# Performance work log

Hardware: AMD Instinct MI355X
Metric: run time of the kernel (lower is better)

## Reference

```python
import jax, jax.numpy as jnp
import numpy as np

N_NODES = 150000
N_ETYPES = 1000
B = 16384
D_CONT = 2
N_NCAT = 3
NCAT_CARD = 64
NCAT_DIM = 16
ETYPE_DIM = 32
N_ECAT = 2
ECAT_CARD = 32
ECAT_DIM = 16
T_DIM = 16
D_IN = D_CONT + N_NCAT * NCAT_DIM      # 50
H = 128                                 # gnn_hidden_dim
P_IN = 2 * H + ETYPE_DIM + N_ECAT * ECAT_DIM + T_DIM  # 336
P_HID = 64


def setup_inputs() -> dict:
    key = jax.random.key(0)
    ks = jax.random.split(key, 24)
    s = 0.05
    inp = {
        "src_node_ids": jax.random.randint(ks[0], (B,), 0, N_NODES),
        "dst_node_ids": jax.random.randint(ks[1], (B,), 0, N_NODES),
        "edge_type_ids": jax.random.randint(ks[2], (B,), 0, N_ETYPES),
        "t_rel": jax.random.uniform(ks[3], (B, 1), dtype=jnp.float32),
        "node_cont": jax.random.normal(ks[4], (N_NODES, D_CONT), dtype=jnp.float32),
        "node_cat_codes": jax.random.randint(ks[5], (N_NCAT, N_NODES), 0, NCAT_CARD),
        "edge_cat_codes": jax.random.randint(ks[6], (N_ECAT, N_ETYPES), 0, ECAT_CARD),
        "edge_index": jax.random.randint(ks[7], (2, 1500000), 0, N_NODES),
        "h_prev": jax.random.normal(ks[8], (N_NODES, H), dtype=jnp.float32),
        "c_prev": jax.random.normal(ks[9], (N_NODES, H), dtype=jnp.float32),
        # learned parameters
        "node_cat_emb": jax.random.normal(ks[10], (N_NCAT, NCAT_CARD, NCAT_DIM), dtype=jnp.float32) * s,
        "edge_id_emb": jax.random.normal(ks[11], (N_ETYPES, ETYPE_DIM), dtype=jnp.float32) * s,
        "edge_cat_emb": jax.random.normal(ks[12], (N_ECAT, ECAT_CARD, ECAT_DIM), dtype=jnp.float32) * s,
        "time_W": jax.random.normal(ks[13], (1, T_DIM), dtype=jnp.float32) * s,
        "time_b": jnp.zeros((T_DIM,), dtype=jnp.float32),
        # GConvLSTM (ChebConv K=1 per gate): gates ordered [i, f, c, o]
        "Wx": jax.random.normal(ks[14], (4, D_IN, H), dtype=jnp.float32) * s,
        "Wh": jax.random.normal(ks[15], (4, H, H), dtype=jnp.float32) * s,
        "b_gate": jnp.zeros((4, H), dtype=jnp.float32),
        "w_c": jax.random.normal(ks[16], (3, H), dtype=jnp.float32) * s,  # peephole for i, f, o
        "W1": jax.random.normal(ks[17], (P_IN, P_HID), dtype=jnp.float32) * s,
        "b1": jnp.zeros((P_HID,), dtype=jnp.float32),
        "W2": jax.random.normal(ks[18], (P_HID, 1), dtype=jnp.float32) * s,
        "b2": jnp.zeros((1,), dtype=jnp.float32),
    }
    return inp


def reference(src_node_ids, dst_node_ids, edge_type_ids, t_rel, node_cont,
              node_cat_codes, edge_cat_codes, edge_index, h_prev, c_prev,
              node_cat_emb, edge_id_emb, edge_cat_emb, time_W, time_b,
              Wx, Wh, b_gate, w_c, W1, b1, W2, b2):
    # --- process node features: cont + 3 categorical embedding gathers ---
    # node_cat_emb[f, node_cat_codes[f, n]] -> [N_NCAT, N, NCAT_DIM]
    cat_e = node_cat_emb[jnp.arange(N_NCAT)[:, None], node_cat_codes]
    cat_e = jnp.transpose(cat_e, (1, 0, 2)).reshape(N_NODES, N_NCAT * NCAT_DIM)
    x = jnp.concatenate([node_cont, cat_e], axis=-1)  # [N, D_IN]

    # --- process batch edge-type features ---
    eid_e = edge_id_emb[edge_type_ids]                               # [B, 32]
    codes_b = edge_cat_codes[:, edge_type_ids]                       # [N_ECAT, B]
    ecat_e = edge_cat_emb[jnp.arange(N_ECAT)[:, None], codes_b]      # [N_ECAT, B, 16]
    ecat_e = jnp.transpose(ecat_e, (1, 0, 2)).reshape(-1, N_ECAT * ECAT_DIM)
    edge_feat = jnp.concatenate([eid_e, ecat_e], axis=-1)            # [B, 64]

    # --- time encoding ---
    t = t_rel if t_rel.ndim == 2 else t_rel[:, None]
    time_e = t @ time_W + time_b                                     # [B, 16]

    # --- GConvLSTM step. ChebConv with K=1: out = x @ W0 + b (T_0(L)x = x),
    # so edge_index is mathematically unused. Gates: [i, f, c_tilde, o]. ---
    z = (jnp.einsum('nd,gdh->gnh', x, Wx)
         + jnp.einsum('nh,ghk->gnk', h_prev, Wh)
         + b_gate[:, None, :])                                       # [4, N, H]
    i_g = jax.nn.sigmoid(z[0] + w_c[0] * c_prev)
    f_g = jax.nn.sigmoid(z[1] + w_c[1] * c_prev)
    t_g = jnp.tanh(z[2])
    c_new = f_g * c_prev + i_g * t_g
    o_g = jax.nn.sigmoid(z[3] + w_c[2] * c_new)
    h_new = o_g * jnp.tanh(c_new)

    # --- link predictor ---
    src_e = h_new[src_node_ids]                                      # [B, H]
    dst_e = h_new[dst_node_ids]                                      # [B, H]
    comb = jnp.concatenate([src_e, dst_e, edge_feat, time_e], axis=-1)  # [B, 336]
    hid = jax.nn.relu(comb @ W1 + b1)
    prob = jax.nn.sigmoid(hid @ W2 + b2)[:, 0]                       # [B]
    return prob, h_new, c_new
```

## Files before the change

### kernel.cpp

```cpp
#include <hip/hip_runtime.h>

#define N_NODES   150000
#define N_PAD     150016
#define B_EDGES   16384
#define H         128
#define KP        192
#define N_NCAT    3
#define NCAT_CARD 64
#define NCAT_DIM  16
#define N_ETYPES  1000
#define ETYPE_DIM 32
#define N_ECAT    2
#define ECAT_CARD 32
#define ECAT_DIM  16
#define T_DIM     16
#define P_IN      336
#define P_HID     64

typedef __bf16 bf16x8 __attribute__((ext_vector_type(8)));
typedef float  f32x4  __attribute__((ext_vector_type(4)));

__device__ __forceinline__ float rcp_(float x)      { return __builtin_amdgcn_rcpf(x); }
__device__ __forceinline__ float sigmoidf_(float x) { return rcp_(1.0f + __expf(-x)); }
__device__ __forceinline__ float tanhf_(float x)    { return 1.0f - 2.0f * rcp_(__expf(2.0f * x) + 1.0f); }
__device__ __forceinline__ unsigned short f2bf(float f) {
    unsigned u = __float_as_uint(f);
    u += 0x7fffu + ((u >> 16) & 1u);
    return (unsigned short)(u >> 16);
}

__global__ __launch_bounds__(256) void build_a_kernel(
    const float* __restrict__ node_cont,
    const int*   __restrict__ node_cat_codes,
    const float* __restrict__ node_cat_emb,
    const float* __restrict__ h_prev,
    unsigned short* __restrict__ A)
{
    const int t = threadIdx.x;
    const int r = t >> 5, l32 = t & 31;
    const int n = blockIdx.x * 8 + r;
    if (n >= N_PAD) return;
    unsigned short* arow = A + (size_t)n * KP;
    #pragma unroll
    for (int s = 0; s < 6; ++s) {
        int j = s * 32 + l32;
        float v = 0.0f;
        if (n < N_NODES) {
            if (j < 2) {
                v = node_cont[n * 2 + j];
            } else if (j < 50) {
                int c = (j - 2) >> 4, d = (j - 2) & 15;
                int code = node_cat_codes[c * N_NODES + n];
                v = node_cat_emb[(c * NCAT_CARD + code) * NCAT_DIM + d];
            } else if (j < 178) {
                v = h_prev[n * H + (j - 50)];
            }
        }
        arow[j] = f2bf(v);
    }
}

__global__ __launch_bounds__(192) void build_w_kernel(
    const float* __restrict__ Wx, const float* __restrict__ Wh,
    unsigned short* __restrict__ Wt)
{
    const int c = blockIdx.x, k = threadIdx.x;
    const int m16 = c & 15;
    const int g   = (c >> 4) & 3;
    const int w   = (c >> 6) & 3;
    const int cbh = c >> 8;
    const int h   = cbh * 64 + w * 16 + m16;
    float v = 0.0f;
    if (k < 50)       v = Wx[(g * 50 + k) * H + h];
    else if (k < 178) v = Wh[(g * H + (k - 50)) * H + h];
    Wt[c * KP + k] = f2bf(v);
}

__global__ __launch_bounds__(256) void lstm_mfma_kernel(
    const unsigned short* __restrict__ A,
    const unsigned short* __restrict__ Wt,
    const float* __restrict__ c_prev,
    const float* __restrict__ b_gate,
    const float* __restrict__ w_c,
    float* __restrict__ h_out,
    float* __restrict__ c_out)
{
    const int t    = threadIdx.x;
    const int wv   = t >> 6, ln = t & 63;
    const int quad = ln >> 4, m16 = ln & 15;
    const int cb   = blockIdx.x;
    const int nb   = blockIdx.y;
    const int nbase = nb * 64;
    const int h     = cb * 64 + wv * 16 + m16;

    const unsigned short* aptr[4];
    const unsigned short* wptr[4];
    #pragma unroll
    for (int mi = 0; mi < 4; ++mi)
        aptr[mi] = A + (size_t)(nbase + mi * 16 + m16) * KP + quad * 8;
    const int cwave = cb * 256 + wv * 64;
    #pragma unroll
    for (int ni = 0; ni < 4; ++ni)
        wptr[ni] = Wt + (size_t)(cwave + ni * 16 + m16) * KP + quad * 8;

    float cpv[4][4];
    #pragma unroll
    for (int mi = 0; mi < 4; ++mi)
        #pragma unroll
        for (int r = 0; r < 4; ++r) {
            int node = nbase + mi * 16 + quad * 4 + r;
            cpv[mi][r] = (node < N_NODES) ? c_prev[(size_t)node * H + h] : 0.0f;
        }

    f32x4 acc[4][4];
    #pragma unroll
    for (int i = 0; i < 4; ++i)
        #pragma unroll
        for (int j = 0; j < 4; ++j) acc[i][j] = (f32x4){0.f, 0.f, 0.f, 0.f};

    #pragma unroll
    for (int kc = 0; kc < 6; ++kc) {
        bf16x8 af[4], bf[4];
        #pragma unroll
        for (int mi = 0; mi < 4; ++mi)
            af[mi] = *(const bf16x8*)(aptr[mi] + kc * 32);
        #pragma unroll
        for (int ni = 0; ni < 4; ++ni)
            bf[ni] = *(const bf16x8*)(wptr[ni] + kc * 32);
        #pragma unroll
        for (int mi = 0; mi < 4; ++mi)
            #pragma unroll
            for (int ni = 0; ni < 4; ++ni)
                acc[mi][ni] = __builtin_amdgcn_mfma_f32_16x16x32_bf16(
                    af[mi], bf[ni], acc[mi][ni], 0, 0, 0);
    }

    const float bg0 = b_gate[0 * H + h], bg1 = b_gate[1 * H + h];
    const float bg2 = b_gate[2 * H + h], bg3 = b_gate[3 * H + h];
    const float wc0 = w_c[0 * H + h], wc1 = w_c[1 * H + h], wc2 = w_c[2 * H + h];

    #pragma unroll
    for (int mi = 0; mi < 4; ++mi)
        #pragma unroll
        for (int r = 0; r < 4; ++r) {
            int node = nbase + mi * 16 + quad * 4 + r;
            if (node < N_NODES) {
                size_t off = (size_t)node * H + h;
                float cp = cpv[mi][r];
                float ig = sigmoidf_(acc[mi][0][r] + bg0 + wc0 * cp);
                float fg = sigmoidf_(acc[mi][1][r] + bg1 + wc1 * cp);
                float tg = tanhf_(acc[mi][2][r] + bg2);
                float cn = fg * cp + ig * tg;
                float og = sigmoidf_(acc[mi][3][r] + bg3 + wc2 * cn);
                h_out[off] = og * tanhf_(cn);
                c_out[off] = cn;
            }
        }
}

__global__ __launch_bounds__(256) void edge_kernel(
    const int*   __restrict__ src,
    const int*   __restrict__ dst,
    const int*   __restrict__ et,
    const float* __restrict__ t_rel,
    const int*   __restrict__ edge_cat_codes,
    const float* __restrict__ edge_id_emb,
    const float* __restrict__ edge_cat_emb,
    const float* __restrict__ time_W,
    const float* __restrict__ time_b,
    const float* __restrict__ W1,
    const float* __restrict__ b1,
    const float* __restrict__ W2,
    const float* __restrict__ b2,
    const float* __restrict__ h_new,
    float* __restrict__ prob)
{
    __shared__ __align__(16) float comb[4][P_IN];
    const int t = threadIdx.x;
    const int el = t >> 6;
    const int j  = t & 63;
    const int e  = blockIdx.x * 4 + el;

    if (e < B_EDGES) {
        const int s = src[e], d = dst[e], ety = et[e];
        comb[el][j]       = h_new[(size_t)s * H + j];
        comb[el][64 + j]  = h_new[(size_t)s * H + 64 + j];
        comb[el][128 + j] = h_new[(size_t)d * H + j];
        comb[el][192 + j] = h_new[(size_t)d * H + 64 + j];
        if (j < 32) {
            comb[el][256 + j] = edge_id_emb[ety * ETYPE_DIM + j];
            int c = j >> 4, dd = j & 15;
            int code = edge_cat_codes[c * N_ETYPES + ety];
            comb[el][288 + j] = edge_cat_emb[(c * ECAT_CARD + code) * ECAT_DIM + dd];
        }
        if (j < T_DIM) comb[el][320 + j] = t_rel[e] * time_W[j] + time_b[j];
    }
    __syncthreads();
    if (e >= B_EDGES) return;

    float h0 = b1[j], h1 = 0.f, h2 = 0.f, h3 = 0.f;
    #pragma unroll 4
    for (int k = 0; k < P_IN; k += 4) {
        float4 cv = *(const float4*)&comb[el][k];
        h0 = fmaf(cv.x, W1[(k + 0) * P_HID + j], h0);
        h1 = fmaf(cv.y, W1[(k + 1) * P_HID + j], h1);
        h2 = fmaf(cv.z, W1[(k + 2) * P_HID + j], h2);
        h3 = fmaf(cv.w, W1[(k + 3) * P_HID + j], h3);
    }
    float hid = fmaxf((h0 + h1) + (h2 + h3), 0.0f);

    float v = hid * W2[j];
    #pragma unroll
    for (int off = 32; off > 0; off >>= 1) v += __shfl_down(v, off);
    if (j == 0) prob[e] = sigmoidf_(v + b2[0]);
}

extern "C" void kernel_launch(void* const* d_in, const int* in_sizes, int n_in,
                              void* d_out, int out_size, void* d_ws, size_t ws_size,
                              hipStream_t stream) {
    const int*   src            = (const int*)  d_in[0];
    const int*   dst            = (const int*)  d_in[1];
    const int*   et             = (const int*)  d_in[2];
    const float* t_rel          = (const float*)d_in[3];
    const float* node_cont      = (const float*)d_in[4];
    const int*   node_cat_codes = (const int*)  d_in[5];
    const int*   edge_cat_codes = (const int*)  d_in[6];
    const float* h_prev         = (const float*)d_in[8];
    const float* c_prev         = (const float*)d_in[9];
    const float* node_cat_emb   = (const float*)d_in[10];
    const float* edge_id_emb    = (const float*)d_in[11];
    const float* edge_cat_emb   = (const float*)d_in[12];
    const float* time_W         = (const float*)d_in[13];
    const float* time_b         = (const float*)d_in[14];
    const float* Wx             = (const float*)d_in[15];
    const float* Wh             = (const float*)d_in[16];
    const float* b_gate         = (const float*)d_in[17];
    const float* w_c            = (const float*)d_in[18];
    const float* W1             = (const float*)d_in[19];
    const float* b1             = (const float*)d_in[20];
    const float* W2             = (const float*)d_in[21];
    const float* b2             = (const float*)d_in[22];

    float* out   = (float*)d_out;
    float* prob  = out;
    float* h_out = out + B_EDGES;
    float* c_out = out + B_EDGES + (size_t)N_NODES * H;

    unsigned short* A  = (unsigned short*)d_ws;
    unsigned short* Wt = (unsigned short*)((char*)d_ws + (size_t)N_PAD * KP * 2);

    build_a_kernel<<<N_PAD / 8, 256, 0, stream>>>(node_cont, node_cat_codes,
                                                  node_cat_emb, h_prev, A);
    build_w_kernel<<<512, 192, 0, stream>>>(Wx, Wh, Wt);

    dim3 grid(2, N_PAD / 64);
    lstm_mfma_kernel<<<grid, 256, 0, stream>>>(A, Wt, c_prev, b_gate, w_c,
                                               h_out, c_out);

    edge_kernel<<<B_EDGES / 4, 256, 0, stream>>>(src, dst, et, t_rel,
                                                 edge_cat_codes, edge_id_emb, edge_cat_emb,
                                                 time_W, time_b, W1, b1, W2, b2,
                                                 h_out, prob);
}
```

Baseline: 517.9 us.

## Fuse bf16 A-matrix construction into LSTM MFMA kernel via swizzled LDS tile

New measurement: 477.9 us. 1.08x faster.

```diff
diff --git a/kernel.cpp b/kernel.cpp
--- a/kernel.cpp
+++ b/kernel.cpp
@@ -19,6 +19,7 @@
 
 typedef __bf16 bf16x8 __attribute__((ext_vector_type(8)));
 typedef float  f32x4  __attribute__((ext_vector_type(4)));
+typedef unsigned int u32x4 __attribute__((ext_vector_type(4)));
 
 __device__ __forceinline__ float rcp_(float x)      { return __builtin_amdgcn_rcpf(x); }
 __device__ __forceinline__ float sigmoidf_(float x) { return rcp_(1.0f + __expf(-x)); }
@@ -27,37 +28,6 @@
     unsigned u = __float_as_uint(f);
     u += 0x7fffu + ((u >> 16) & 1u);
     return (unsigned short)(u >> 16);
-}
-
-__global__ __launch_bounds__(256) void build_a_kernel(
-    const float* __restrict__ node_cont,
-    const int*   __restrict__ node_cat_codes,
-    const float* __restrict__ node_cat_emb,
-    const float* __restrict__ h_prev,
-    unsigned short* __restrict__ A)
-{
-    const int t = threadIdx.x;
-    const int r = t >> 5, l32 = t & 31;
-    const int n = blockIdx.x * 8 + r;
-    if (n >= N_PAD) return;
-    unsigned short* arow = A + (size_t)n * KP;
-    #pragma unroll
-    for (int s = 0; s < 6; ++s) {
-        int j = s * 32 + l32;
-        float v = 0.0f;
-        if (n < N_NODES) {
-            if (j < 2) {
-                v = node_cont[n * 2 + j];
-            } else if (j < 50) {
-                int c = (j - 2) >> 4, d = (j - 2) & 15;
-                int code = node_cat_codes[c * N_NODES + n];
-                v = node_cat_emb[(c * NCAT_CARD + code) * NCAT_DIM + d];
-            } else if (j < 178) {
-                v = h_prev[n * H + (j - 50)];
-            }
-        }
-        arow[j] = f2bf(v);
-    }
 }
 
 __global__ __launch_bounds__(192) void build_w_kernel(
@@ -76,8 +46,11 @@
     Wt[c * KP + k] = f2bf(v);
 }
 
-__global__ __launch_bounds__(256) void lstm_mfma_kernel(
-    const unsigned short* __restrict__ A,
+__global__ __launch_bounds__(512, 4) void lstm_mfma_fused(
+    const float* __restrict__ node_cont,
+    const int*   __restrict__ node_cat_codes,
+    const float* __restrict__ node_cat_emb,
+    const float* __restrict__ h_prev,
     const unsigned short* __restrict__ Wt,
     const float* __restrict__ c_prev,
     const float* __restrict__ b_gate,
@@ -85,32 +58,57 @@
     float* __restrict__ h_out,
     float* __restrict__ c_out)
 {
-    const int t    = threadIdx.x;
+    __shared__ __align__(16) unsigned short Asub[6 * 64 * 32];
+
+    const int t     = threadIdx.x;
+    const int nbase = blockIdx.x * 64;
+
+    {
+        const int brow  = t >> 3;
+        const int bsub  = t & 7;
+        const int bnode = nbase + brow;
+        const bool valid = bnode < N_NODES;
+        #pragma unroll
+        for (int s = 0; s < 3; ++s) {
+            const int at = bsub + s * 8;
+            const int j0 = at * 8;
+            float v[8];
+            #pragma unroll
+            for (int e = 0; e < 8; ++e) {
+                const int j = j0 + e;
+                float x = 0.0f;
+                if (valid) {
+                    if (j < 2) {
+                        x = node_cont[bnode * 2 + j];
+                    } else if (j < 50) {
+                        int c = (j - 2) >> 4, d = (j - 2) & 15;
+                        int code = node_cat_codes[c * N_NODES + bnode];
+                        x = node_cat_emb[(c * NCAT_CARD + code) * NCAT_DIM + d];
+                    } else if (j < 178) {
+                        x = h_prev[(size_t)bnode * H + (j - 50)];
+                    }
+                }
+                v[e] = x;
+            }
+            unsigned u[4];
+            #pragma unroll
+            for (int p = 0; p < 4; ++p)
+                u[p] = (unsigned)f2bf(v[2 * p]) | ((unsigned)f2bf(v[2 * p + 1]) << 16);
+            const int kc = at >> 2, a = at & 3;
+            const int as = a ^ ((brow >> 1) & 3);
+            *(u32x4*)&Asub[(kc * 64 + brow) * 32 + as * 8] = *(const u32x4*)u;
+        }
+    }
+    __syncthreads();
+
     const int wv   = t >> 6, ln = t & 63;
     const int quad = ln >> 4, m16 = ln & 15;
-    const int cb   = blockIdx.x;
-    const int nb   = blockIdx.y;
-    const int nbase = nb * 64;
-    const int h     = cb * 64 + wv * 16 + m16;
-
-    const unsigned short* aptr[4];
+    const int h    = (wv >> 2) * 64 + (wv & 3) * 16 + m16;
+
     const unsigned short* wptr[4];
     #pragma unroll
-    for (int mi = 0; mi < 4; ++mi)
-        aptr[mi] = A + (size_t)(nbase + mi * 16 + m16) * KP + quad * 8;
-    const int cwave = cb * 256 + wv * 64;
-    #pragma unroll
     for (int ni = 0; ni < 4; ++ni)
-        wptr[ni] = Wt + (size_t)(cwave + ni * 16 + m16) * KP + quad * 8;
-
-    float cpv[4][4];
-    #pragma unroll
-    for (int mi = 0; mi < 4; ++mi)
-        #pragma unroll
-        for (int r = 0; r < 4; ++r) {
-            int node = nbase + mi * 16 + quad * 4 + r;
-            cpv[mi][r] = (node < N_NODES) ? c_prev[(size_t)node * H + h] : 0.0f;
-        }
+        wptr[ni] = Wt + (size_t)(wv * 64 + ni * 16 + m16) * KP + quad * 8;
 
     f32x4 acc[4][4];
     #pragma unroll
@@ -122,8 +120,11 @@
     for (int kc = 0; kc < 6; ++kc) {
         bf16x8 af[4], bf[4];
         #pragma unroll
-        for (int mi = 0; mi < 4; ++mi)
-            af[mi] = *(const bf16x8*)(aptr[mi] + kc * 32);
+        for (int mi = 0; mi < 4; ++mi) {
+            const int row = mi * 16 + m16;
+            const int as  = quad ^ ((row >> 1) & 3);
+            af[mi] = *(const bf16x8*)&Asub[(kc * 64 + row) * 32 + as * 8];
+        }
         #pragma unroll
         for (int ni = 0; ni < 4; ++ni)
             bf[ni] = *(const bf16x8*)(wptr[ni] + kc * 32);
@@ -143,10 +144,10 @@
     for (int mi = 0; mi < 4; ++mi)
         #pragma unroll
         for (int r = 0; r < 4; ++r) {
-            int node = nbase + mi * 16 + quad * 4 + r;
+            const int node = nbase + mi * 16 + quad * 4 + r;
             if (node < N_NODES) {
-                size_t off = (size_t)node * H + h;
-                float cp = cpv[mi][r];
+                const size_t off = (size_t)node * H + h;
+                const float cp = c_prev[off];
                 float ig = sigmoidf_(acc[mi][0][r] + bg0 + wc0 * cp);
                 float fg = sigmoidf_(acc[mi][1][r] + bg1 + wc1 * cp);
                 float tg = tanhf_(acc[mi][2][r] + bg2);
@@ -246,16 +247,13 @@
     float* h_out = out + B_EDGES;
     float* c_out = out + B_EDGES + (size_t)N_NODES * H;
 
-    unsigned short* A  = (unsigned short*)d_ws;
-    unsigned short* Wt = (unsigned short*)((char*)d_ws + (size_t)N_PAD * KP * 2);
-
-    build_a_kernel<<<N_PAD / 8, 256, 0, stream>>>(node_cont, node_cat_codes,
-                                                  node_cat_emb, h_prev, A);
+    unsigned short* Wt = (unsigned short*)d_ws;
+
     build_w_kernel<<<512, 192, 0, stream>>>(Wx, Wh, Wt);
 
-    dim3 grid(2, N_PAD / 64);
-    lstm_mfma_kernel<<<grid, 256, 0, stream>>>(A, Wt, c_prev, b_gate, w_c,
-                                               h_out, c_out);
+    lstm_mfma_fused<<<N_PAD / 64, 512, 0, stream>>>(
+        node_cont, node_cat_codes, node_cat_emb, h_prev, Wt, c_prev,
+        b_gate, w_c, h_out, c_out);
 
     edge_kernel<<<B_EDGES / 4, 256, 0, stream>>>(src, dst, et, t_rel,
                                                  edge_cat_codes, edge_id_emb, edge_cat_emb,
```
